# Performance work log

Hardware: AMD Instinct MI355X
Metric: run time of the kernel (lower is better)

Reference implementation:

```python
import jax, jax.numpy as jnp
import numpy as np

B, S, D, H = 2, 2048, 2048, 16
HD = D // H  # head_dim = 128
ALIBI_BIAS_MAX = 8


def alibi_bias(n_heads, seq_len, alibi_bias_max=8, dtype=jnp.float32):
    # matches torch alibi_bias(full=False): shape [1, H, 1, S]
    dist = jnp.arange(1 - seq_len, 1, dtype=dtype).reshape(1, 1, 1, seq_len)
    m = jnp.arange(1, n_heads + 1, dtype=dtype) * (alibi_bias_max / n_heads)
    slopes = (1.0 / 2.0 ** m).reshape(1, n_heads, 1, 1)
    return dist * slopes


def setup_inputs() -> dict:
    key = jax.random.key(0)
    k1, k2, k3, k4, k5 = jax.random.split(key, 5)
    x = jax.random.normal(k1, (B, S, D), dtype=jnp.float32)
    # ALiBi additive bias, as produced by TritonFlashCausalAttention.attn_mask_
    attn_mask = alibi_bias(H, S, ALIBI_BIAS_MAX, jnp.float32)  # [1,H,1,S]
    scale = 1.0 / np.sqrt(D)
    Wqkv = jax.random.normal(k2, (D, 3 * D), dtype=jnp.float32) * scale
    bqkv = jnp.zeros((3 * D,), dtype=jnp.float32)
    Wout = jax.random.normal(k3, (D, D), dtype=jnp.float32) * scale
    bout = jnp.zeros((D,), dtype=jnp.float32)
    return {"x": x, "attn_mask": attn_mask, "Wqkv": Wqkv, "bqkv": bqkv,
            "Wout": Wout, "bout": bout}


def reference(x, attn_mask, Wqkv, bqkv, Wout, bout):
    b, s, d = x.shape
    # fused QKV projection
    qkv = x @ Wqkv + bqkv                       # [B,S,3D]
    qkv = qkv.reshape(b, s, 3, H, HD)
    q, k, v = qkv[:, :, 0], qkv[:, :, 1], qkv[:, :, 2]  # each [B,S,H,HD]
    softmax_scale = 1.0 / jnp.sqrt(jnp.asarray(HD, dtype=x.dtype))
    scores = jnp.einsum('bshd,bthd->bhst', q, k) * softmax_scale  # [B,H,S,S]
    scores = scores + attn_mask                  # ALiBi bias [1,H,1,S]
    causal = jnp.tril(jnp.ones((s, s), dtype=bool))
    scores = jnp.where(causal, scores, jnp.asarray(-jnp.inf, dtype=scores.dtype))
    attn = jax.nn.softmax(scores, axis=-1)
    out = jnp.einsum('bhst,bthd->bshd', attn, v).reshape(b, s, d)
    return out @ Wout + bout
```

## Files before the change

### kernel.cpp

```cpp
#include <hip/hip_runtime.h>
#include <hip/hip_bf16.h>

typedef __bf16 bf16x8 __attribute__((ext_vector_type(8)));
typedef float f32x4 __attribute__((ext_vector_type(4)));
typedef unsigned short u16;

constexpr int BATCH = 2, SEQ = 2048, DM = 2048, NH = 16, HD = 128;
constexpr int N3 = 3 * DM;
constexpr int MROWS = BATCH * SEQ;

__device__ __forceinline__ u16 f2bf(float f) {
  unsigned u = __builtin_bit_cast(unsigned, f);
  unsigned r = 0x7FFFu + ((u >> 16) & 1u);
  return (u16)((u + r) >> 16);
}

__device__ __forceinline__ void glds16(const u16* g, u16* l) {
  __builtin_amdgcn_global_load_lds(
      (const __attribute__((address_space(1))) unsigned*)(const void*)g,
      (__attribute__((address_space(3))) unsigned*)(void*)l, 16, 0, 0);
}

__global__ __launch_bounds__(256) void k_cvt(const float* __restrict__ in,
                                             u16* __restrict__ out, int n4) {
  int i = blockIdx.x * blockDim.x + threadIdx.x;
  if (i >= n4) return;
  float4 v = reinterpret_cast<const float4*>(in)[i];
  ushort4 o;
  o.x = f2bf(v.x); o.y = f2bf(v.y); o.z = f2bf(v.z); o.w = f2bf(v.w);
  reinterpret_cast<ushort4*>(out)[i] = o;
}

__global__ __launch_bounds__(256) void k_transpose(const float* __restrict__ in,
                                                   u16* __restrict__ out, int K, int N) {
  __shared__ float tile[32][33];
  int n0 = blockIdx.x * 32, k0 = blockIdx.y * 32;
  int tx = threadIdx.x & 31, ty = threadIdx.x >> 5;
#pragma unroll
  for (int r = ty; r < 32; r += 8) tile[r][tx] = in[(long)(k0 + r) * N + n0 + tx];
  __syncthreads();
#pragma unroll
  for (int r = ty; r < 32; r += 8) out[(long)(n0 + r) * K + k0 + tx] = f2bf(tile[tx][r]);
}

__global__ __launch_bounds__(256, 2) void k_gemm_qkv(const u16* __restrict__ A,
                                                     const u16* __restrict__ Bt,
                                                     const float* __restrict__ bias,
                                                     u16* __restrict__ Qb, u16* __restrict__ Kb,
                                                     u16* __restrict__ Vt) {
  constexpr int K = DM;
  constexpr int NKT = K / 64;
  constexpr int NIT = NKT / 2;
  __shared__ u16 LA[2 * 128 * 64];
  __shared__ u16 LB[2 * 192 * 64];
  int lin = blockIdx.y * 32 + blockIdx.x;
  int wid = (lin & 7) * 128 + (lin >> 3);
  int m0 = (wid & 31) * 128;
  int n0 = (wid >> 5) * 192;
  int t = threadIdx.x, lane = t & 63, w = t >> 6;
  int l15 = lane & 15, lhi = lane >> 4;
  int wrow = w >> 1, wcol = w & 1;
  int srow = t >> 3;
  int scol = ((t & 7) ^ (srow & 7)) * 8;

#define STG_A(TILE, IDX) do {                                                      \
    int kb_ = ((TILE) < NKT ? (TILE) : NKT - 1) * 64;                              \
    glds16(A + (long)(m0 + (IDX) * 32 + srow) * K + kb_ + scol,                    \
           LA + ((TILE) & 1) * 8192 + (IDX) * 2048 + w * 512);                     \
  } while (0)
#define STG_B(TILE, IDX) do {                                                      \
    int kb_ = ((TILE) < NKT ? (TILE) : NKT - 1) * 64;                              \
    glds16(Bt + (long)(n0 + (IDX) * 32 + srow) * K + kb_ + scol,                   \
           LB + ((TILE) & 1) * 12288 + (IDX) * 2048 + w * 512);                    \
  } while (0)

  bf16x8 af[2][2], bfr0[3][2], bfr1[3][2];
  f32x4 acc[4][6] = {};

#define LDA_FRAGS(BUF, QM) do {                                                    \
    _Pragma("unroll") for (int mi = 0; mi < 2; mi++) {                             \
      int rA = wrow * 64 + ((QM) * 2 + mi) * 16 + l15;                             \
      _Pragma("unroll") for (int kk = 0; kk < 2; kk++)                             \
        af[mi][kk] = *(const bf16x8*)(LA + (BUF) * 8192 + rA * 64 +                \
                                      (((kk * 4 + lhi) ^ (rA & 7)) * 8));          \
    } } while (0)
#define LDB_FRAGS(BUF, QN, DST) do {                                               \
    _Pragma("unroll") for (int ni = 0; ni < 3; ni++) {                             \
      int rB = wcol * 96 + ((QN) * 3 + ni) * 16 + l15;                             \
      _Pragma("unroll") for (int kk = 0; kk < 2; kk++)                             \
        DST[ni][kk] = *(const bf16x8*)(LB + (BUF) * 12288 + rB * 64 +              \
                                       (((kk * 4 + lhi) ^ (rB & 7)) * 8));         \
    } } while (0)
#define MM(QM, QN, BF) do {                                                        \
    __builtin_amdgcn_s_setprio(1);                                                 \
    _Pragma("unroll") for (int mi = 0; mi < 2; mi++)                               \
    _Pragma("unroll") for (int ni = 0; ni < 3; ni++)                               \
    _Pragma("unroll") for (int kk = 0; kk < 2; kk++)                               \
      acc[(QM) * 2 + mi][(QN) * 3 + ni] = __builtin_amdgcn_mfma_f32_16x16x32_bf16( \
          af[mi][kk], BF[ni][kk], acc[(QM) * 2 + mi][(QN) * 3 + ni], 0, 0, 0);     \
    __builtin_amdgcn_s_setprio(0);                                                 \
  } while (0)
#define BAR __builtin_amdgcn_s_barrier()
#define LG0 do { asm volatile("s_waitcnt lgkmcnt(0)" ::: "memory");                \
                 __builtin_amdgcn_sched_barrier(0); } while (0)
#define VMW6 do { asm volatile("s_waitcnt vmcnt(6)" ::: "memory");                 \
                  __builtin_amdgcn_sched_barrier(0); } while (0)

  STG_A(0, 0); STG_A(0, 1); STG_A(0, 2); STG_A(0, 3);
  STG_B(0, 0); STG_B(0, 1); STG_B(0, 2); STG_B(0, 3); STG_B(0, 4); STG_B(0, 5);
  STG_B(1, 0); STG_B(1, 1); STG_B(1, 2); STG_B(1, 3); STG_B(1, 4); STG_B(1, 5);
  VMW6; BAR;

  for (int it = 0; it < NIT; it++) {
    int k1 = 2 * it + 1, k2 = 2 * it + 2, k3 = 2 * it + 3;
    LDA_FRAGS(0, 0); LDB_FRAGS(0, 0, bfr0);
    STG_A(k1, 0); STG_A(k1, 1); STG_A(k1, 2);      BAR; LG0; MM(0, 0, bfr0); BAR;
    LDB_FRAGS(0, 1, bfr1);
    STG_A(k1, 3);                                  BAR; LG0; MM(0, 1, bfr1); BAR;
    LDA_FRAGS(0, 1);
    STG_B(k2, 0); STG_B(k2, 1); STG_B(k2, 2);      BAR; LG0; MM(1, 0, bfr0); BAR;
    STG_B(k2, 3); STG_B(k2, 4); STG_B(k2, 5);
    VMW6;                                          BAR;      MM(1, 1, bfr1); BAR;
    LDA_FRAGS(1, 0); LDB_FRAGS(1, 0, bfr0);
    STG_A(k2, 0); STG_A(k2, 1); STG_A(k2, 2);      BAR; LG0; MM(0, 0, bfr0); BAR;
    LDB_FRAGS(1, 1, bfr1);
    STG_A(k2, 3);                                  BAR; LG0; MM(0, 1, bfr1); BAR;
    LDA_FRAGS(1, 1);
    STG_B(k3, 0); STG_B(k3, 1); STG_B(k3, 2);      BAR; LG0; MM(1, 0, bfr0); BAR;
    STG_B(k3, 3); STG_B(k3, 4); STG_B(k3, 5);
    VMW6;                                          BAR;      MM(1, 1, bfr1); BAR;
  }
#undef STG_A
#undef STG_B
#undef LDA_FRAGS
#undef LDB_FRAGS
#undef MM
#undef BAR
#undef LG0
#undef VMW6

#pragma unroll
  for (int mi = 0; mi < 4; mi++)
#pragma unroll
    for (int ni = 0; ni < 6; ni++) {
      int col = n0 + wcol * 96 + ni * 16 + l15;
      float bv = bias[col];
      int sec = col >> 11, dn = col & 2047, h = dn >> 7, hd = dn & 127;
#pragma unroll
      for (int r = 0; r < 4; r++) {
        int row = m0 + wrow * 64 + mi * 16 + lhi * 4 + r;
        int bb = row >> 11, ss = row & 2047;
        u16 val = f2bf(acc[mi][ni][r] + bv);
        if (sec == 0)
          Qb[(((long)(bb * NH + h)) * SEQ + ss) * HD + hd] = val;
        else if (sec == 1)
          Kb[(((long)(bb * NH + h)) * SEQ + ss) * HD + hd] = val;
        else
          Vt[(((long)(bb * NH + h)) * HD + hd) * SEQ + ss] = val;
      }
    }
}

__global__ __launch_bounds__(256, 2) void k_gemm_out(const u16* __restrict__ A,
                                                     const u16* __restrict__ Bt,
                                                     const float* __restrict__ bias,
                                                     float* __restrict__ Out) {
  constexpr int K = DM, N = DM;
  constexpr int NKT = K / 64;
  constexpr int NIT = NKT / 2;
  __shared__ u16 LA[2 * 128 * 64];
  __shared__ u16 LB[2 * 128 * 64];
  int lin = blockIdx.y * 16 + blockIdx.x;
  int wid = (lin & 7) * 64 + (lin >> 3);
  int m0 = (wid & 31) * 128;
  int n0 = (wid >> 5) * 128;
  int t = threadIdx.x, lane = t & 63, w = t >> 6;
  int l15 = lane & 15, lhi = lane >> 4;
  int wrow = w >> 1, wcol = w & 1;
  int srow = t >> 3;
  int scol = ((t & 7) ^ (srow & 7)) * 8;

#define STG_A(TILE, IDX) do {                                                      \
    int kb_ = ((TILE) < NKT ? (TILE) : NKT - 1) * 64;                              \
    glds16(A + (long)(m0 + (IDX) * 32 + srow) * K + kb_ + scol,                    \
           LA + ((TILE) & 1) * 8192 + (IDX) * 2048 + w * 512);                     \
  } while (0)
#define STG_B(TILE, IDX) do {                                                      \
    int kb_ = ((TILE) < NKT ? (TILE) : NKT - 1) * 64;                              \
    glds16(Bt + (long)(n0 + (IDX) * 32 + srow) * K + kb_ + scol,                   \
           LB + ((TILE) & 1) * 8192 + (IDX) * 2048 + w * 512);                     \
  } while (0)

  bf16x8 af[2][2], bfr0[2][2], bfr1[2][2];
  f32x4 acc[4][4] = {};

#define LDA_FRAGS(BUF, QM) do {                                                    \
    _Pragma("unroll") for (int mi = 0; mi < 2; mi++) {                             \
      int rA = wrow * 64 + ((QM) * 2 + mi) * 16 + l15;                             \
      _Pragma("unroll") for (int kk = 0; kk < 2; kk++)                             \
        af[mi][kk] = *(const bf16x8*)(LA + (BUF) * 8192 + rA * 64 +                \
                                      (((kk * 4 + lhi) ^ (rA & 7)) * 8));          \
    } } while (0)
#define LDB_FRAGS(BUF, QN, DST) do {                                               \
    _Pragma("unroll") for (int ni = 0; ni < 2; ni++) {                             \
      int rB = wcol * 64 + ((QN) * 2 + ni) * 16 + l15;                             \
      _Pragma("unroll") for (int kk = 0; kk < 2; kk++)                             \
        DST[ni][kk] = *(const bf16x8*)(LB + (BUF) * 8192 + rB * 64 +               \
                                       (((kk * 4 + lhi) ^ (rB & 7)) * 8));         \
    } } while (0)
#define MM(QM, QN, BF) do {                                                        \
    __builtin_amdgcn_s_setprio(1);                                                 \
    _Pragma("unroll") for (int mi = 0; mi < 2; mi++)                               \
    _Pragma("unroll") for (int ni = 0; ni < 2; ni++)                               \
    _Pragma("unroll") for (int kk = 0; kk < 2; kk++)                               \
      acc[(QM) * 2 + mi][(QN) * 2 + ni] = __builtin_amdgcn_mfma_f32_16x16x32_bf16( \
          af[mi][kk], BF[ni][kk], acc[(QM) * 2 + mi][(QN) * 2 + ni], 0, 0, 0);     \
    __builtin_amdgcn_s_setprio(0);                                                 \
  } while (0)
#define BAR __builtin_amdgcn_s_barrier()
#define LG0 do { asm volatile("s_waitcnt lgkmcnt(0)" ::: "memory");                \
                 __builtin_amdgcn_sched_barrier(0); } while (0)
#define VMW4 do { asm volatile("s_waitcnt vmcnt(4)" ::: "memory");                 \
                  __builtin_amdgcn_sched_barrier(0); } while (0)

  STG_A(0, 0); STG_A(0, 1); STG_A(0, 2); STG_A(0, 3);
  STG_B(0, 0); STG_B(0, 1); STG_B(0, 2); STG_B(0, 3);
  STG_B(1, 0); STG_B(1, 1); STG_B(1, 2); STG_B(1, 3);
  VMW4; BAR;

  for (int it = 0; it < NIT; it++) {
    int k1 = 2 * it + 1, k2 = 2 * it + 2, k3 = 2 * it + 3;
    LDA_FRAGS(0, 0); LDB_FRAGS(0, 0, bfr0);
    STG_A(k1, 0); STG_A(k1, 1); STG_A(k1, 2);      BAR; LG0; MM(0, 0, bfr0); BAR;
    LDB_FRAGS(0, 1, bfr1);
    STG_A(k1, 3);                                  BAR; LG0; MM(0, 1, bfr1); BAR;
    LDA_FRAGS(0, 1);
    STG_B(k2, 0); STG_B(k2, 1); STG_B(k2, 2);      BAR; LG0; MM(1, 0, bfr0); BAR;
    STG_B(k2, 3);
    VMW4;                                          BAR;      MM(1, 1, bfr1); BAR;
    LDA_FRAGS(1, 0); LDB_FRAGS(1, 0, bfr0);
    STG_A(k2, 0); STG_A(k2, 1); STG_A(k2, 2);      BAR; LG0; MM(0, 0, bfr0); BAR;
    LDB_FRAGS(1, 1, bfr1);
    STG_A(k2, 3);                                  BAR; LG0; MM(0, 1, bfr1); BAR;
    LDA_FRAGS(1, 1);
    STG_B(k3, 0); STG_B(k3, 1); STG_B(k3, 2);      BAR; LG0; MM(1, 0, bfr0); BAR;
    STG_B(k3, 3);
    VMW4;                                          BAR;      MM(1, 1, bfr1); BAR;
  }
#undef STG_A
#undef STG_B
#undef LDA_FRAGS
#undef LDB_FRAGS
#undef MM
#undef BAR
#undef LG0
#undef VMW4

#pragma unroll
  for (int mi = 0; mi < 4; mi++)
#pragma unroll
    for (int ni = 0; ni < 4; ni++) {
      int col = n0 + wcol * 64 + ni * 16 + l15;
      float bv = bias[col];
#pragma unroll
      for (int r = 0; r < 4; r++) {
        int row = m0 + wrow * 64 + mi * 16 + lhi * 4 + r;
        Out[(long)row * N + col] = acc[mi][ni][r] + bv;
      }
    }
}

__global__ __launch_bounds__(256) void k_attn(const u16* __restrict__ Qb,
                                              const u16* __restrict__ Kb,
                                              const u16* __restrict__ Vt,
                                              const float* __restrict__ mask,
                                              u16* __restrict__ Ao) {
  constexpr int NT = SEQ / 64;
  int lin = blockIdx.y * gridDim.x + blockIdx.x;
  int wid = (lin & 7) * 64 + (lin >> 3);
  int bh = wid >> 4;
  int qp = wid & 15;
  int t = threadIdx.x, w = t >> 6, lane = t & 63;
  int l15 = lane & 15, lhi = lane >> 4;
  int b = bh >> 4, h = bh & 15;
  const u16* Qh = Qb + (long)bh * SEQ * HD;
  const u16* Kh = Kb + (long)bh * SEQ * HD;
  const u16* Vh = Vt + (long)bh * HD * SEQ;
  const float* mh = mask + h * SEQ;

  __shared__ u16 Ks[64 * 128];
  __shared__ u16 Vs[128 * 64];
  __shared__ u16 p_lds[4 * 16 * 64];
  u16* pw = p_lds + w * (16 * 64);

  int krow[4], kcol[4], vrow[4], vcol[4];
#pragma unroll
  for (int i = 0; i < 4; i++) {
    int c = i * 256 + t;
    krow[i] = c >> 4; kcol[i] = (c & 15) * 8;
    vrow[i] = c >> 3; vcol[i] = (c & 7) * 8;
  }

  const float sm_scale = 0.08838834764831845f;

  for (int half = 0; half < 2; half++) {
    int qt = half ? qp : (NT - 1 - qp);
    int q0 = qt * 64 + w * 16;
    int nt = qt + 1;

    bf16x8 qf[4];
#pragma unroll
    for (int kc = 0; kc < 4; kc++)
      qf[kc] = *(const bf16x8*)(Qh + (long)(q0 + l15) * HD + kc * 32 + lhi * 8);

    int rowr[4];
#pragma unroll
    for (int r = 0; r < 4; r++) rowr[r] = q0 + lhi * 4 + r;

    float mrun[4], lrun[4];
    f32x4 oacc[8] = {};
#pragma unroll
    for (int r = 0; r < 4; r++) { mrun[r] = -1e30f; lrun[r] = 0.f; }

    bf16x8 kst[4], vst[4];
#pragma unroll
    for (int i = 0; i < 4; i++) kst[i] = *(const bf16x8*)(Kh + (long)krow[i] * HD + kcol[i]);
#pragma unroll
    for (int i = 0; i < 4; i++) vst[i] = *(const bf16x8*)(Vh + (long)vrow[i] * SEQ + vcol[i]);
    __syncthreads();
#pragma unroll
    for (int i = 0; i < 4; i++)
      *(bf16x8*)(Ks + krow[i] * 128 + (kcol[i] ^ ((krow[i] & 7) << 3))) = kst[i];
#pragma unroll
    for (int i = 0; i < 4; i++)
      *(bf16x8*)(Vs + vrow[i] * 64 + (vcol[i] ^ ((vrow[i] & 7) << 3))) = vst[i];
    __syncthreads();

    for (int kt = 0; kt < nt; kt++) {
      int kb = kt * 64;
      bool have_next = (kt + 1 < nt);
      bool diag = (kt == nt - 1);
      if (have_next) {
        int kb2 = kb + 64;
#pragma unroll
        for (int i = 0; i < 4; i++)
          kst[i] = *(const bf16x8*)(Kh + (long)(kb2 + krow[i]) * HD + kcol[i]);
#pragma unroll
        for (int i = 0; i < 4; i++)
          vst[i] = *(const bf16x8*)(Vh + (long)vrow[i] * SEQ + kb2 + vcol[i]);
      }
      float bvv[4];
#pragma unroll
      for (int cb = 0; cb < 4; cb++) bvv[cb] = mh[kb + cb * 16 + l15];
      f32x4 sc[4] = {};
      __builtin_amdgcn_s_setprio(1);
#pragma unroll
      for (int kc = 0; kc < 4; kc++)
#pragma unroll
        for (int cb = 0; cb < 4; cb++) {
          int rr = cb * 16 + l15;
          bf16x8 kf = *(const bf16x8*)(Ks + rr * 128 + ((kc * 32 + lhi * 8) ^ ((rr & 7) << 3)));
          sc[cb] = __builtin_amdgcn_mfma_f32_16x16x32_bf16(qf[kc], kf, sc[cb], 0, 0, 0);
        }
      __builtin_amdgcn_s_setprio(0);
      float p[4][4], tmax[4];
#pragma unroll
      for (int cb = 0; cb < 4; cb++) {
        int col = kb + cb * 16 + l15;
#pragma unroll
        for (int r = 0; r < 4; r++) {
          float v = sc[cb][r] * sm_scale + bvv[cb];
          if (diag) v = (col <= rowr[r]) ? v : -1e30f;
          p[cb][r] = v;
        }
      }
#pragma unroll
      for (int r = 0; r < 4; r++)
        tmax[r] = fmaxf(fmaxf(p[0][r], p[1][r]), fmaxf(p[2][r], p[3][r]));
      float alpha[4];
#pragma unroll
      for (int r = 0; r < 4; r++) {
        float v = tmax[r];
        v = fmaxf(v, __shfl_xor(v, 1));
        v = fmaxf(v, __shfl_xor(v, 2));
        v = fmaxf(v, __shfl_xor(v, 4));
        v = fmaxf(v, __shfl_xor(v, 8));
        float mnew = fmaxf(mrun[r], v);
        alpha[r] = __expf(mrun[r] - mnew);
        mrun[r] = mnew;
        float s = 0.f;
#pragma unroll
        for (int cb = 0; cb < 4; cb++) {
          float e = __expf(p[cb][r] - mnew);
          p[cb][r] = e;
          s += e;
        }
        s += __shfl_xor(s, 1); s += __shfl_xor(s, 2);
        s += __shfl_xor(s, 4); s += __shfl_xor(s, 8);
        lrun[r] = lrun[r] * alpha[r] + s;
      }
#pragma unroll
      for (int nb = 0; nb < 8; nb++)
#pragma unroll
        for (int r = 0; r < 4; r++) oacc[nb][r] *= alpha[r];
#pragma unroll
      for (int cb = 0; cb < 4; cb++)
#pragma unroll
        for (int r = 0; r < 4; r++) {
          int rr = lhi * 4 + r;
          pw[(rr * 64 + cb * 16 + l15) ^ ((rr & 7) << 3)] = f2bf(p[cb][r]);
        }
      asm volatile("s_waitcnt lgkmcnt(0)" ::: "memory");
      bf16x8 pa0 = *(const bf16x8*)(pw + ((l15 * 64 + lhi * 8) ^ ((l15 & 7) << 3)));
      bf16x8 pa1 = *(const bf16x8*)(pw + ((l15 * 64 + 32 + lhi * 8) ^ ((l15 & 7) << 3)));
      __builtin_amdgcn_s_setprio(1);
#pragma unroll
      for (int nb = 0; nb < 8; nb++) {
        int rr = nb * 16 + l15;
        bf16x8 vf0 = *(const bf16x8*)(Vs + rr * 64 + ((lhi * 8) ^ ((rr & 7) << 3)));
        bf16x8 vf1 = *(const bf16x8*)(Vs + rr * 64 + ((32 + lhi * 8) ^ ((rr & 7) << 3)));
        oacc[nb] = __builtin_amdgcn_mfma_f32_16x16x32_bf16(pa0, vf0, oacc[nb], 0, 0, 0);
        oacc[nb] = __builtin_amdgcn_mfma_f32_16x16x32_bf16(pa1, vf1, oacc[nb], 0, 0, 0);
      }
      __builtin_amdgcn_s_setprio(0);
      if (have_next) {
        __syncthreads();
#pragma unroll
        for (int i = 0; i < 4; i++)
          *(bf16x8*)(Ks + krow[i] * 128 + (kcol[i] ^ ((krow[i] & 7) << 3))) = kst[i];
#pragma unroll
        for (int i = 0; i < 4; i++)
          *(bf16x8*)(Vs + vrow[i] * 64 + (vcol[i] ^ ((vrow[i] & 7) << 3))) = vst[i];
        __syncthreads();
      }
    }
#pragma unroll
    for (int nb = 0; nb < 8; nb++)
#pragma unroll
      for (int r = 0; r < 4; r++) {
        int row = q0 + lhi * 4 + r;
        float v = oacc[nb][r] / lrun[r];
        Ao[((long)(b * SEQ + row)) * DM + h * HD + nb * 16 + l15] = f2bf(v);
      }
  }
}

extern "C" void kernel_launch(void* const* d_in, const int* in_sizes, int n_in,
                              void* d_out, int out_size, void* d_ws, size_t ws_size,
                              hipStream_t stream) {
  const float* x    = (const float*)d_in[0];
  const float* amsk = (const float*)d_in[1];
  const float* Wqkv = (const float*)d_in[2];
  const float* bqkv = (const float*)d_in[3];
  const float* Wout = (const float*)d_in[4];
  const float* bout = (const float*)d_in[5];
  float* out = (float*)d_out;

  char* ws = (char*)d_ws;
  u16* xb  = (u16*)(ws + 0);
  u16* WqT = (u16*)(ws + 16777216UL);
  u16* WoT = (u16*)(ws + 41943040UL);
  u16* Qb  = (u16*)(ws + 50331648UL);
  u16* Kb  = (u16*)(ws + 67108864UL);
  u16* Vt  = (u16*)(ws + 83886080UL);
  u16* Ao  = (u16*)(ws + 100663296UL);

  k_cvt<<<8192, 256, 0, stream>>>(x, xb, (MROWS * DM) / 4);
  k_transpose<<<dim3(N3 / 32, DM / 32), 256, 0, stream>>>(Wqkv, WqT, DM, N3);
  k_transpose<<<dim3(DM / 32, DM / 32), 256, 0, stream>>>(Wout, WoT, DM, DM);
  k_gemm_qkv<<<dim3(32, 32), 256, 0, stream>>>(xb, WqT, bqkv, Qb, Kb, Vt);
  k_attn<<<dim3(SEQ / 128, BATCH * NH), 256, 0, stream>>>(Qb, Kb, Vt, amsk, Ao);
  k_gemm_out<<<dim3(16, 32), 256, 0, stream>>>(Ao, WoT, bout, out);
}
```

Baseline: 339.9 us.

## Double-buffer K/V tiles in attention via direct global-to-LDS loads

Replaces the register-staged K/V prefetch with global_load_lds DMA into double-buffered shared memory. The swizzle is moved onto the global source addresses, and the two barriers per iteration become one. The block-to-work remap is also dropped in favour of direct blockIdx mapping, which changes L2 locality and scheduling order. The aim is to free VGPRs and overlap the loads with compute, at the cost of doubling LDS use, which may lower occupancy. It also relies on the direct-to-LDS loads being complete at the barrier, with no explicit vmcnt wait.

```diff
diff --git a/kernel.cpp b/kernel.cpp
--- a/kernel.cpp
+++ b/kernel.cpp
@@ -276,10 +276,8 @@
                                               const float* __restrict__ mask,
                                               u16* __restrict__ Ao) {
   constexpr int NT = SEQ / 64;
-  int lin = blockIdx.y * gridDim.x + blockIdx.x;
-  int wid = (lin & 7) * 64 + (lin >> 3);
-  int bh = wid >> 4;
-  int qp = wid & 15;
+  int bh = blockIdx.y;
+  int qp = blockIdx.x;
   int t = threadIdx.x, w = t >> 6, lane = t & 63;
   int l15 = lane & 15, lhi = lane >> 4;
   int b = bh >> 4, h = bh & 15;
@@ -288,18 +286,28 @@
   const u16* Vh = Vt + (long)bh * HD * SEQ;
   const float* mh = mask + h * SEQ;
 
-  __shared__ u16 Ks[64 * 128];
-  __shared__ u16 Vs[128 * 64];
+  __shared__ u16 Ks[2][64 * 128];
+  __shared__ u16 Vs[2][128 * 64];
   __shared__ u16 p_lds[4 * 16 * 64];
   u16* pw = p_lds + w * (16 * 64);
 
-  int krow[4], kcol[4], vrow[4], vcol[4];
+  int krow[4], kcolS[4], vrow[4], vcolS[4];
 #pragma unroll
   for (int i = 0; i < 4; i++) {
     int c = i * 256 + t;
-    krow[i] = c >> 4; kcol[i] = (c & 15) * 8;
-    vrow[i] = c >> 3; vcol[i] = (c & 7) * 8;
+    krow[i] = c >> 4; kcolS[i] = ((c & 15) ^ ((c >> 4) & 7)) * 8;
+    vrow[i] = c >> 3; vcolS[i] = ((c & 7) ^ ((c >> 3) & 7)) * 8;
   }
+
+#define STAGE(KT, BUF) do {                                                        \
+    int kb_ = (KT) * 64;                                                           \
+    _Pragma("unroll") for (int i = 0; i < 4; i++)                                  \
+      glds16(Kh + (long)(kb_ + krow[i]) * HD + kcolS[i],                           \
+             &Ks[BUF][(i * 256 + w * 64) * 8]);                                    \
+    _Pragma("unroll") for (int i = 0; i < 4; i++)                                  \
+      glds16(Vh + (long)vrow[i] * SEQ + kb_ + vcolS[i],                            \
+             &Vs[BUF][(i * 256 + w * 64) * 8]);                                    \
+  } while (0)
 
   const float sm_scale = 0.08838834764831845f;
 
@@ -322,33 +330,16 @@
 #pragma unroll
     for (int r = 0; r < 4; r++) { mrun[r] = -1e30f; lrun[r] = 0.f; }
 
-    bf16x8 kst[4], vst[4];
-#pragma unroll
-    for (int i = 0; i < 4; i++) kst[i] = *(const bf16x8*)(Kh + (long)krow[i] * HD + kcol[i]);
-#pragma unroll
-    for (int i = 0; i < 4; i++) vst[i] = *(const bf16x8*)(Vh + (long)vrow[i] * SEQ + vcol[i]);
+    STAGE(0, 0);
     __syncthreads();
-#pragma unroll
-    for (int i = 0; i < 4; i++)
-      *(bf16x8*)(Ks + krow[i] * 128 + (kcol[i] ^ ((krow[i] & 7) << 3))) = kst[i];
-#pragma unroll
-    for (int i = 0; i < 4; i++)
-      *(bf16x8*)(Vs + vrow[i] * 64 + (vcol[i] ^ ((vrow[i] & 7) << 3))) = vst[i];
-    __syncthreads();
 
     for (int kt = 0; kt < nt; kt++) {
+      int cur = kt & 1;
+      if (kt + 1 < nt) STAGE(kt + 1, cur ^ 1);
+      bool diag = (kt == nt - 1);
       int kb = kt * 64;
-      bool have_next = (kt + 1 < nt);
-      bool diag = (kt == nt - 1);
-      if (have_next) {
-        int kb2 = kb + 64;
-#pragma unroll
-        for (int i = 0; i < 4; i++)
-          kst[i] = *(const bf16x8*)(Kh + (long)(kb2 + krow[i]) * HD + kcol[i]);
-#pragma unroll
-        for (int i = 0; i < 4; i++)
-          vst[i] = *(const bf16x8*)(Vh + (long)vrow[i] * SEQ + kb2 + vcol[i]);
-      }
+      const u16* Ksg = Ks[cur];
+      const u16* Vsg = Vs[cur];
       float bvv[4];
 #pragma unroll
       for (int cb = 0; cb < 4; cb++) bvv[cb] = mh[kb + cb * 16 + l15];
@@ -359,7 +350,7 @@
 #pragma unroll
         for (int cb = 0; cb < 4; cb++) {
           int rr = cb * 16 + l15;
-          bf16x8 kf = *(const bf16x8*)(Ks + rr * 128 + ((kc * 32 + lhi * 8) ^ ((rr & 7) << 3)));
+          bf16x8 kf = *(const bf16x8*)(Ksg + rr * 128 + ((kc * 32 + lhi * 8) ^ ((rr & 7) << 3)));
           sc[cb] = __builtin_amdgcn_mfma_f32_16x16x32_bf16(qf[kc], kf, sc[cb], 0, 0, 0);
         }
       __builtin_amdgcn_s_setprio(0);
@@ -417,22 +408,13 @@
 #pragma unroll
       for (int nb = 0; nb < 8; nb++) {
         int rr = nb * 16 + l15;
-        bf16x8 vf0 = *(const bf16x8*)(Vs + rr * 64 + ((lhi * 8) ^ ((rr & 7) << 3)));
-        bf16x8 vf1 = *(const bf16x8*)(Vs + rr * 64 + ((32 + lhi * 8) ^ ((rr & 7) << 3)));
+        bf16x8 vf0 = *(const bf16x8*)(Vsg + rr * 64 + ((lhi * 8) ^ ((rr & 7) << 3)));
+        bf16x8 vf1 = *(const bf16x8*)(Vsg + rr * 64 + ((32 + lhi * 8) ^ ((rr & 7) << 3)));
         oacc[nb] = __builtin_amdgcn_mfma_f32_16x16x32_bf16(pa0, vf0, oacc[nb], 0, 0, 0);
         oacc[nb] = __builtin_amdgcn_mfma_f32_16x16x32_bf16(pa1, vf1, oacc[nb], 0, 0, 0);
       }
       __builtin_amdgcn_s_setprio(0);
-      if (have_next) {
-        __syncthreads();
-#pragma unroll
-        for (int i = 0; i < 4; i++)
-          *(bf16x8*)(Ks + krow[i] * 128 + (kcol[i] ^ ((krow[i] & 7) << 3))) = kst[i];
-#pragma unroll
-        for (int i = 0; i < 4; i++)
-          *(bf16x8*)(Vs + vrow[i] * 64 + (vcol[i] ^ ((vrow[i] & 7) << 3))) = vst[i];
-        __syncthreads();
-      }
+      __syncthreads();
     }
 #pragma unroll
     for (int nb = 0; nb < 8; nb++)
@@ -443,6 +425,7 @@
         Ao[((long)(b * SEQ + row)) * DM + h * HD + nb * 16 + l15] = f2bf(v);
       }
   }
+#undef STAGE
 }
 
 extern "C" void kernel_launch(void* const* d_in, const int* in_sizes, int n_in,
```

Measured after the change: 294.6 us. 1.15x faster.
